# Kernel optimization log

Hardware: AMD Instinct MI355X
Metric: run time of the kernel (lower is better)

The kernel has to match this reference:

```python
import jax, jax.numpy as jnp
import numpy as np

DEGREE = 3
N_KNOTS = 5

def _bspline_basis(x, t_ext, degree):
    """Vectorized Cox-de Boor. x: (..., ), t_ext: (m,) extended knots.
    Returns (..., m-1-degree) degree-`degree` basis values."""
    xe = x[..., None]
    # order-0 indicator basis: (..., m-1)
    B = ((xe >= t_ext[:-1]) & (xe < t_ext[1:])).astype(x.dtype)
    for p in range(1, degree + 1):
        left_den = t_ext[p:-1] - t_ext[:-(p + 1)]
        right_den = t_ext[p + 1:] - t_ext[1:-p]
        left = jnp.where(left_den > 0,
                         (xe - t_ext[:-(p + 1)]) / jnp.where(left_den > 0, left_den, 1.0),
                         0.0) * B[..., :-1]
        right = jnp.where(right_den > 0,
                          (t_ext[p + 1:] - xe) / jnp.where(right_den > 0, right_den, 1.0),
                          0.0) * B[..., 1:]
        B = left + right
    return B

def setup_inputs() -> dict:
    key = jax.random.key(0)
    k1, k2, k3, k4 = jax.random.split(key, 4)
    batch, input_dim, out_dim = 16384, 4096, 64
    n_coeff = N_KNOTS - DEGREE  # 2
    return {
        "x": jax.random.normal(k1, (batch, input_dim), dtype=jnp.float32),
        "c": jax.random.normal(k2, (input_dim, out_dim, n_coeff), dtype=jnp.float32),
        "ws": jax.random.normal(k3, (input_dim, out_dim), dtype=jnp.float32),
        "wb": jax.random.normal(k4, (input_dim, out_dim), dtype=jnp.float32),
    }

def reference(x, c, ws, wb):
    t = jnp.linspace(-1.0, 1.0, N_KNOTS, dtype=x.dtype)
    t_ext = jnp.concatenate([t, t[-1:]])  # pad so basis count == n_knots - degree
    # B: (batch, input_dim, n_coeff); basis depends only on x, shared knots
    B = _bspline_basis(x, t_ext, DEGREE)
    spline = jnp.einsum('bik,ijk->bj', B, c * ws[:, :, None])
    silu_mix = jax.nn.silu(x) @ wb  # sum_i wb[i,j] * x_i*sigmoid(x_i)
    return spline + silu_mix
```

## Files before the change

kernel.cpp:

```cpp
#include <hip/hip_runtime.h>
#include <hip/hip_bf16.h>
#include <stdint.h>

#define BATCH   16384
#define IN_DIM  4096
#define OUT_DIM 64
#define KI      64
#define KCH     (3*KI)
#define NCHUNK  (IN_DIM/KI)
#define SPLITK  4
#define CPB     (NCHUNK/SPLITK)
#define MTILES  (BATCH/64)
#define CHW     (OUT_DIM*KCH)

typedef __attribute__((ext_vector_type(8))) short   short8;
typedef __attribute__((ext_vector_type(4))) float   floatx4;
typedef __attribute__((ext_vector_type(4))) uint32_t uintx4;

static __device__ __forceinline__ unsigned short f2bf(float f) {
    union { float f; uint32_t u; } v; v.f = f;
    uint32_t r = v.u + 0x7FFFu + ((v.u >> 16) & 1u);
    return (unsigned short)(r >> 16);
}

static __device__ __forceinline__ uint32_t pk2bf(float lo, float hi) {
    union { float f; uint32_t u; } a, b;
    a.f = lo; b.f = hi;
    uint32_t ra = a.u + 0x7FFFu + ((a.u >> 16) & 1u);
    uint32_t rb = b.u + 0x7FFFu + ((b.u >> 16) & 1u);
    return (ra >> 16) | (rb & 0xFFFF0000u);
}

static __device__ __forceinline__ void kan_features(float xv, float& b0, float& b1, float& sl) {
    float ax = fabsf(xv);
    float a2 = ax*ax;
    float om = 1.0f - ax;
    float inner = __builtin_fmaf(__builtin_fmaf(4.0f, ax, -4.0f), a2, (2.0f/3.0f));
    float outer = (om*om) * (om * (4.0f/3.0f));
    b0 = (ax < 0.5f) ? inner : outer;
    b0 = (ax < 1.0f) ? b0 : 0.0f;
    float c3  = (xv < 0.0f) ? (4.0f/3.0f) : (-14.0f/3.0f);
    float mid = __builtin_fmaf(__builtin_fmaf(__builtin_fmaf(c3, xv, 2.0f), xv, 1.0f), xv, (1.0f/6.0f));
    float hi  = __builtin_fmaf(__builtin_fmaf(__builtin_fmaf(22.0f, xv, -48.0f), xv, 30.0f), xv, -4.0f) * (1.0f/3.0f);
    b1 = (xv < 0.5f) ? mid : hi;
    b1 = (xv >= -0.5f && xv < 1.0f) ? b1 : 0.0f;
    float e = __expf(-xv);
    sl = xv * __builtin_amdgcn_rcpf(1.0f + e);
}

__global__ __launch_bounds__(256) void kan_prep(
        const float* __restrict__ c, const float* __restrict__ ws,
        const float* __restrict__ wb, unsigned short* __restrict__ Wt) {
    int idx = blockIdx.x * 256 + threadIdx.x;
    int row = idx >> 9;
    int i   = (idx & 511) << 3;
    int j   = row / 3;
    int t   = row - j*3;
    int ci  = i >> 6, il0 = i & 63;
    unsigned short pk[8];
    #pragma unroll
    for (int e = 0; e < 8; e++) {
        int ii = i + e;
        float v;
        if (t < 2) v = c[(size_t)ii*(OUT_DIM*2) + j*2 + t] * ws[(size_t)ii*OUT_DIM + j];
        else       v = wb[(size_t)ii*OUT_DIM + j];
        pk[e] = f2bf(v);
    }
    uintx4 d;
    d[0] = pk[0] | ((uint32_t)pk[1] << 16);
    d[1] = pk[2] | ((uint32_t)pk[3] << 16);
    d[2] = pk[4] | ((uint32_t)pk[5] << 16);
    d[3] = pk[6] | ((uint32_t)pk[7] << 16);
    int g = j*24 + (((t << 3) | (il0 >> 3)) ^ (j & 7));
    *(uintx4*)(Wt + (size_t)ci*CHW + g*8) = d;
}

__global__ __launch_bounds__(256, 4) void kan_main_pre(
    const float* __restrict__ x, const unsigned short* __restrict__ Wt,
    float* __restrict__ pbuf)
{
    __shared__ unsigned short Bs[CHW];

    const int tid  = threadIdx.x;
    const int wave = tid >> 6;
    const int lane = tid & 63;
    const int m    = lane & 15;
    const int q    = lane >> 4;
    const int mt   = blockIdx.x & (MTILES - 1);
    const int kh   = blockIdx.x >> 8;
    const int row0 = mt * 64;
    const int r    = row0 + wave*16 + m;
    const float* xrow = x + (size_t)r * IN_DIM;

    floatx4 acc[4] = {};

    const int i00 = kh * CPB * KI;
    floatx4 xv[4];
    xv[0] = *(const floatx4*)(xrow + i00 + q*8);
    xv[1] = *(const floatx4*)(xrow + i00 + q*8 + 4);
    xv[2] = *(const floatx4*)(xrow + i00 + 32 + q*8);
    xv[3] = *(const floatx4*)(xrow + i00 + 32 + q*8 + 4);

    for (int cc = 0; cc < CPB; cc++) {
        const int ci = kh * CPB + cc;
        const int i0 = ci * KI;

        const int inx = (cc + 1 < CPB) ? (i0 + KI) : i0;
        floatx4 xvn[4];
        xvn[0] = *(const floatx4*)(xrow + inx + q*8);
        xvn[1] = *(const floatx4*)(xrow + inx + q*8 + 4);
        xvn[2] = *(const floatx4*)(xrow + inx + 32 + q*8);
        xvn[3] = *(const floatx4*)(xrow + inx + 32 + q*8 + 4);

        uintx4 afu[6];
        #pragma unroll
        for (int g = 0; g < 2; g++) {
            #pragma unroll
            for (int w = 0; w < 4; w++) {
                float v0 = xv[g*2 + (w >> 1)][(w & 1)*2 + 0];
                float v1 = xv[g*2 + (w >> 1)][(w & 1)*2 + 1];
                float b00, b10, sl0, b01, b11, sl1;
                kan_features(v0, b00, b10, sl0);
                kan_features(v1, b01, b11, sl1);
                afu[0 + g][w] = pk2bf(b00, b01);
                afu[2 + g][w] = pk2bf(b10, b11);
                afu[4 + g][w] = pk2bf(sl0, sl1);
            }
        }

        __syncthreads();

        const unsigned short* gW = Wt + (size_t)ci * CHW;
        #pragma unroll
        for (int p = 0; p < 6; p++) {
            int g0 = p*256 + wave*64;
            __builtin_amdgcn_global_load_lds(
                (__attribute__((address_space(1))) void*)(gW + (size_t)(g0 + lane)*8),
                (__attribute__((address_space(3))) void*)(Bs + (size_t)g0*8),
                16, 0, 0);
        }

        __syncthreads();

        #pragma unroll
        for (int s = 0; s < 6; s++) {
            const int kb = (s >> 1)*8 + (s & 1)*4 + q;
            #pragma unroll
            for (int n = 0; n < 4; n++) {
                const int j = n*16 + m;
                short8 bf = *(const short8*)&Bs[j*KCH + ((kb ^ (j & 7)) << 3)];
                acc[n] = __builtin_amdgcn_mfma_f32_16x16x32_bf16(
                    __builtin_bit_cast(short8, afu[s]), bf, acc[n], 0, 0, 0);
            }
        }

        xv[0] = xvn[0]; xv[1] = xvn[1]; xv[2] = xvn[2]; xv[3] = xvn[3];
    }

    float* pb = pbuf + (((size_t)kh*MTILES + mt)*4)*256*4;
    #pragma unroll
    for (int n = 0; n < 4; n++)
        *(floatx4*)(pb + ((size_t)n*256 + tid)*4) = acc[n];
}

__global__ __launch_bounds__(256) void kan_reduce(
    const float* __restrict__ pbuf, float* __restrict__ out)
{
    const int mt   = blockIdx.x;
    const int tid  = threadIdx.x;
    const int wave = tid >> 6;
    const int lane = tid & 63;
    const int m    = lane & 15;
    const int q    = lane >> 4;
    #pragma unroll
    for (int n = 0; n < 4; n++) {
        floatx4 s = {};
        #pragma unroll
        for (int p = 0; p < SPLITK; p++) {
            floatx4 v = *(const floatx4*)(pbuf +
                ((((size_t)p*MTILES + mt)*4 + n)*256 + tid)*4);
            s += v;
        }
        #pragma unroll
        for (int reg = 0; reg < 4; reg++) {
            int orow = mt*64 + wave*16 + q*4 + reg;
            out[(size_t)orow*OUT_DIM + n*16 + m] = s[reg];
        }
    }
}

__global__ __launch_bounds__(256, 4) void kan_main_fb(
    const float* __restrict__ x, const float* __restrict__ c,
    const float* __restrict__ ws, const float* __restrict__ wb,
    float* __restrict__ out)
{
    __shared__ unsigned short Bs[CHW];
    const int tid  = threadIdx.x;
    const int wave = tid >> 6;
    const int lane = tid & 63;
    const int m    = lane & 15;
    const int q    = lane >> 4;
    const int mt   = blockIdx.x & (MTILES - 1);
    const int kh   = blockIdx.x >> 8;
    const int row0 = mt * 64;
    const int r    = row0 + wave*16 + m;
    const float* xrow = x + (size_t)r * IN_DIM;
    floatx4 acc[4] = {};
    for (int cc = 0; cc < CPB; cc++) {
        const int i0 = (kh * CPB + cc) * KI;
        floatx4 xv[4];
        xv[0] = *(const floatx4*)(xrow + i0 + q*8);
        xv[1] = *(const floatx4*)(xrow + i0 + q*8 + 4);
        xv[2] = *(const floatx4*)(xrow + i0 + 32 + q*8);
        xv[3] = *(const floatx4*)(xrow + i0 + 32 + q*8 + 4);
        uintx4 afu[6];
        #pragma unroll
        for (int g = 0; g < 2; g++) {
            #pragma unroll
            for (int w = 0; w < 4; w++) {
                float v0 = xv[g*2 + (w >> 1)][(w & 1)*2 + 0];
                float v1 = xv[g*2 + (w >> 1)][(w & 1)*2 + 1];
                float b00, b10, sl0, b01, b11, sl1;
                kan_features(v0, b00, b10, sl0);
                kan_features(v1, b01, b11, sl1);
                afu[0 + g][w] = pk2bf(b00, b01);
                afu[2 + g][w] = pk2bf(b10, b11);
                afu[4 + g][w] = pk2bf(sl0, sl1);
            }
        }
        __syncthreads();
        #pragma unroll
        for (int p = 0; p < 16; p++) {
            int idx = tid + p*256;
            int j = idx & 63, i = idx >> 6;
            int gi = i0 + i;
            const float* cp = c + ((size_t)gi*OUT_DIM + j)*2;
            float c0 = cp[0], c1 = cp[1];
            float sw = ws[(size_t)gi*OUT_DIM + j];
            float b  = wb[(size_t)gi*OUT_DIM + j];
            int jx = j & 7;
            Bs[j*KCH + ((0*8 + (i>>3)) ^ jx)*8 + (i&7)] = f2bf(c0*sw);
            Bs[j*KCH + ((1*8 + (i>>3)) ^ jx)*8 + (i&7)] = f2bf(c1*sw);
            Bs[j*KCH + ((2*8 + (i>>3)) ^ jx)*8 + (i&7)] = f2bf(b);
        }
        __syncthreads();
        #pragma unroll
        for (int s = 0; s < 6; s++) {
            const int kb = (s >> 1)*8 + (s & 1)*4 + q;
            #pragma unroll
            for (int n = 0; n < 4; n++) {
                const int j = n*16 + m;
                short8 bf = *(const short8*)&Bs[j*KCH + ((kb ^ (j & 7)) << 3)];
                acc[n] = __builtin_amdgcn_mfma_f32_16x16x32_bf16(
                    __builtin_bit_cast(short8, afu[s]), bf, acc[n], 0, 0, 0);
            }
        }
    }
    #pragma unroll
    for (int n = 0; n < 4; n++)
        #pragma unroll
        for (int reg = 0; reg < 4; reg++) {
            int orow = row0 + wave*16 + q*4 + reg;
            atomicAdd(&out[(size_t)orow*OUT_DIM + n*16 + m], acc[n][reg]);
        }
}

extern "C" void kernel_launch(void* const* d_in, const int* in_sizes, int n_in,
                              void* d_out, int out_size, void* d_ws, size_t ws_size,
                              hipStream_t stream) {
    const float* x  = (const float*)d_in[0];
    const float* c  = (const float*)d_in[1];
    const float* ws = (const float*)d_in[2];
    const float* wb = (const float*)d_in[3];
    float* out = (float*)d_out;

    const size_t part_bytes = (size_t)SPLITK * BATCH * OUT_DIM * sizeof(float);
    const size_t wt_bytes   = (size_t)NCHUNK * CHW * sizeof(unsigned short);
    if (ws_size >= part_bytes + wt_bytes) {
        float* pbuf = (float*)d_ws;
        unsigned short* Wt = (unsigned short*)((char*)d_ws + part_bytes);
        kan_prep<<<384, 256, 0, stream>>>(c, ws, wb, Wt);
        kan_main_pre<<<MTILES * SPLITK, 256, 0, stream>>>(x, Wt, pbuf);
        kan_reduce<<<MTILES, 256, 0, stream>>>(pbuf, out);
    } else {
        hipMemsetAsync(d_out, 0, (size_t)out_size * sizeof(float), stream);
        kan_main_fb<<<MTILES * SPLITK, 256, 0, stream>>>(x, c, ws, wb, out);
    }
}
```

Measured before the change: 411.3 us.

## Double-buffer weight chunks via async LDS loads with smaller K-chunks and split-K 8

The main kernel now processes 32-wide input chunks with split-K raised to 8, and double-buffers the pre-packed weight chunk in LDS. The next chunk's global_load_lds is issued before the MFMA work on the current one, leaving one barrier per iteration instead of two. The weight layout uses a padded stride of 13 granules per output column instead of the XOR swizzle, occupancy is raised to 6 blocks, and the basis math clamps inputs rather than adding range selects. The cost is a partial-sum buffer twice as large, a longer reduce, and more blocks.

```diff
diff --git a/kernel.cpp b/kernel.cpp
--- a/kernel.cpp
+++ b/kernel.cpp
@@ -5,12 +5,19 @@
 #define BATCH   16384
 #define IN_DIM  4096
 #define OUT_DIM 64
+#define MTILES  (BATCH/64)
+
+#define KI2     32
+#define NCH2    (IN_DIM/KI2)
+#define SPLITK  8
+#define CPB2    (NCH2/SPLITK)
+#define GRAN2   (OUT_DIM*13)
+#define CH2W    (GRAN2*8)
+
 #define KI      64
 #define KCH     (3*KI)
 #define NCHUNK  (IN_DIM/KI)
-#define SPLITK  4
-#define CPB     (NCHUNK/SPLITK)
-#define MTILES  (BATCH/64)
+#define FCPB    16
 #define CHW     (OUT_DIM*KCH)
 
 typedef __attribute__((ext_vector_type(8))) short   short8;
@@ -32,18 +39,18 @@
 }
 
 static __device__ __forceinline__ void kan_features(float xv, float& b0, float& b1, float& sl) {
-    float ax = fabsf(xv);
-    float a2 = ax*ax;
-    float om = 1.0f - ax;
-    float inner = __builtin_fmaf(__builtin_fmaf(4.0f, ax, -4.0f), a2, (2.0f/3.0f));
+    float ax  = fabsf(xv);
+    float axc = fminf(ax, 1.0f);
+    float a2  = axc*axc;
+    float om  = 1.0f - axc;
+    float inner = __builtin_fmaf(__builtin_fmaf(4.0f, axc, -4.0f), a2, (2.0f/3.0f));
     float outer = (om*om) * (om * (4.0f/3.0f));
-    b0 = (ax < 0.5f) ? inner : outer;
-    b0 = (ax < 1.0f) ? b0 : 0.0f;
-    float c3  = (xv < 0.0f) ? (4.0f/3.0f) : (-14.0f/3.0f);
-    float mid = __builtin_fmaf(__builtin_fmaf(__builtin_fmaf(c3, xv, 2.0f), xv, 1.0f), xv, (1.0f/6.0f));
-    float hi  = __builtin_fmaf(__builtin_fmaf(__builtin_fmaf(22.0f, xv, -48.0f), xv, 30.0f), xv, -4.0f) * (1.0f/3.0f);
-    b1 = (xv < 0.5f) ? mid : hi;
-    b1 = (xv >= -0.5f && xv < 1.0f) ? b1 : 0.0f;
+    b0 = (axc < 0.5f) ? inner : outer;
+    float xc  = fminf(fmaxf(xv, -0.5f), 1.0f);
+    float c3  = (xc < 0.0f) ? (4.0f/3.0f) : (-14.0f/3.0f);
+    float mid = __builtin_fmaf(__builtin_fmaf(__builtin_fmaf(c3, xc, 2.0f), xc, 1.0f), xc, (1.0f/6.0f));
+    float hi  = __builtin_fmaf(__builtin_fmaf(__builtin_fmaf(22.0f, xc, -48.0f), xc, 30.0f), xc, -4.0f) * (1.0f/3.0f);
+    b1 = (xc < 0.5f) ? mid : hi;
     float e = __expf(-xv);
     sl = xv * __builtin_amdgcn_rcpf(1.0f + e);
 }
@@ -56,7 +63,8 @@
     int i   = (idx & 511) << 3;
     int j   = row / 3;
     int t   = row - j*3;
-    int ci  = i >> 6, il0 = i & 63;
+    int ci  = i >> 5;
+    int ig  = (i & 31) >> 3;
     unsigned short pk[8];
     #pragma unroll
     for (int e = 0; e < 8; e++) {
@@ -71,15 +79,15 @@
     d[1] = pk[2] | ((uint32_t)pk[3] << 16);
     d[2] = pk[4] | ((uint32_t)pk[5] << 16);
     d[3] = pk[6] | ((uint32_t)pk[7] << 16);
-    int g = j*24 + (((t << 3) | (il0 >> 3)) ^ (j & 7));
-    *(uintx4*)(Wt + (size_t)ci*CHW + g*8) = d;
-}
-
-__global__ __launch_bounds__(256, 4) void kan_main_pre(
+    int g = j*13 + t*4 + ig;
+    *(uintx4*)(Wt + (size_t)ci*CH2W + (size_t)g*8) = d;
+}
+
+__global__ __launch_bounds__(256, 6) void kan_main_pre(
     const float* __restrict__ x, const unsigned short* __restrict__ Wt,
     float* __restrict__ pbuf)
 {
-    __shared__ unsigned short Bs[CHW];
+    __shared__ unsigned short Bs[2][CH2W];
 
     const int tid  = threadIdx.x;
     const int wave = tid >> 6;
@@ -91,27 +99,140 @@
     const int row0 = mt * 64;
     const int r    = row0 + wave*16 + m;
     const float* xrow = x + (size_t)r * IN_DIM;
+    const int ci0 = kh * CPB2;
 
     floatx4 acc[4] = {};
 
-    const int i00 = kh * CPB * KI;
-    floatx4 xv[4];
-    xv[0] = *(const floatx4*)(xrow + i00 + q*8);
-    xv[1] = *(const floatx4*)(xrow + i00 + q*8 + 4);
-    xv[2] = *(const floatx4*)(xrow + i00 + 32 + q*8);
-    xv[3] = *(const floatx4*)(xrow + i00 + 32 + q*8 + 4);
-
-    for (int cc = 0; cc < CPB; cc++) {
-        const int ci = kh * CPB + cc;
-        const int i0 = ci * KI;
-
-        const int inx = (cc + 1 < CPB) ? (i0 + KI) : i0;
-        floatx4 xvn[4];
-        xvn[0] = *(const floatx4*)(xrow + inx + q*8);
-        xvn[1] = *(const floatx4*)(xrow + inx + q*8 + 4);
-        xvn[2] = *(const floatx4*)(xrow + inx + 32 + q*8);
-        xvn[3] = *(const floatx4*)(xrow + inx + 32 + q*8 + 4);
-
+    floatx4 xv0 = *(const floatx4*)(xrow + ci0*KI2 + q*8);
+    floatx4 xv1 = *(const floatx4*)(xrow + ci0*KI2 + q*8 + 4);
+
+    {
+        const unsigned short* gW = Wt + (size_t)ci0 * CH2W;
+        #pragma unroll
+        for (int p = 0; p < 3; p++) {
+            int g0 = p*256 + wave*64;
+            __builtin_amdgcn_global_load_lds(
+                (__attribute__((address_space(1))) void*)(gW + (size_t)(g0 + lane)*8),
+                (__attribute__((address_space(3))) void*)(&Bs[0][0] + (size_t)g0*8),
+                16, 0, 0);
+        }
+        if (tid < 64)
+            __builtin_amdgcn_global_load_lds(
+                (__attribute__((address_space(1))) void*)(gW + (size_t)(768 + lane)*8),
+                (__attribute__((address_space(3))) void*)(&Bs[0][0] + (size_t)768*8),
+                16, 0, 0);
+    }
+    __syncthreads();
+
+    for (int cc = 0; cc < CPB2; cc++) {
+        const int buf = cc & 1;
+        const int ci  = ci0 + cc;
+
+        if (cc + 1 < CPB2) {
+            const unsigned short* gW = Wt + (size_t)(ci + 1) * CH2W;
+            #pragma unroll
+            for (int p = 0; p < 3; p++) {
+                int g0 = p*256 + wave*64;
+                __builtin_amdgcn_global_load_lds(
+                    (__attribute__((address_space(1))) void*)(gW + (size_t)(g0 + lane)*8),
+                    (__attribute__((address_space(3))) void*)(&Bs[buf^1][0] + (size_t)g0*8),
+                    16, 0, 0);
+            }
+            if (tid < 64)
+                __builtin_amdgcn_global_load_lds(
+                    (__attribute__((address_space(1))) void*)(gW + (size_t)(768 + lane)*8),
+                    (__attribute__((address_space(3))) void*)(&Bs[buf^1][0] + (size_t)768*8),
+                    16, 0, 0);
+        }
+
+        const int inx = (cc + 1 < CPB2) ? (ci + 1)*KI2 : ci*KI2;
+        floatx4 xn0 = *(const floatx4*)(xrow + inx + q*8);
+        floatx4 xn1 = *(const floatx4*)(xrow + inx + q*8 + 4);
+
+        uintx4 afu[3];
+        #pragma unroll
+        for (int w = 0; w < 4; w++) {
+            float v0 = (w < 2) ? xv0[w*2]     : xv1[(w-2)*2];
+            float v1 = (w < 2) ? xv0[w*2 + 1] : xv1[(w-2)*2 + 1];
+            float b00, b10, s0, b01, b11, s1;
+            kan_features(v0, b00, b10, s0);
+            kan_features(v1, b01, b11, s1);
+            afu[0][w] = pk2bf(b00, b01);
+            afu[1][w] = pk2bf(b10, b11);
+            afu[2][w] = pk2bf(s0, s1);
+        }
+
+        #pragma unroll
+        for (int t = 0; t < 3; t++) {
+            #pragma unroll
+            for (int n = 0; n < 4; n++) {
+                const int j = n*16 + m;
+                short8 bf = *(const short8*)&Bs[buf][(size_t)(j*13 + t*4 + q)*8];
+                acc[n] = __builtin_amdgcn_mfma_f32_16x16x32_bf16(
+                    __builtin_bit_cast(short8, afu[t]), bf, acc[n], 0, 0, 0);
+            }
+        }
+
+        xv0 = xn0; xv1 = xn1;
+        __syncthreads();
+    }
+
+    float* pb = pbuf + (((size_t)kh*MTILES + mt)*4)*1024;
+    #pragma unroll
+    for (int n = 0; n < 4; n++)
+        *(floatx4*)(pb + ((size_t)n*256 + tid)*4) = acc[n];
+}
+
+__global__ __launch_bounds__(256) void kan_reduce(
+    const float* __restrict__ pbuf, float* __restrict__ out)
+{
+    const int mt   = blockIdx.x;
+    const int tid  = threadIdx.x;
+    const int wave = tid >> 6;
+    const int lane = tid & 63;
+    const int m    = lane & 15;
+    const int q    = lane >> 4;
+    #pragma unroll
+    for (int n = 0; n < 4; n++) {
+        floatx4 s = {};
+        #pragma unroll
+        for (int p = 0; p < SPLITK; p++) {
+            floatx4 v = *(const floatx4*)(pbuf +
+                (((size_t)p*MTILES + mt)*4 + n)*1024 + (size_t)tid*4);
+            s += v;
+        }
+        #pragma unroll
+        for (int reg = 0; reg < 4; reg++) {
+            int orow = mt*64 + wave*16 + q*4 + reg;
+            out[(size_t)orow*OUT_DIM + n*16 + m] = s[reg];
+        }
+    }
+}
+
+__global__ __launch_bounds__(256, 4) void kan_main_fb(
+    const float* __restrict__ x, const float* __restrict__ c,
+    const float* __restrict__ ws, const float* __restrict__ wb,
+    float* __restrict__ out)
+{
+    __shared__ unsigned short Bsf[CHW];
+    const int tid  = threadIdx.x;
+    const int wave = tid >> 6;
+    const int lane = tid & 63;
+    const int m    = lane & 15;
+    const int q    = lane >> 4;
+    const int mt   = blockIdx.x & (MTILES - 1);
+    const int kh   = blockIdx.x >> 8;
+    const int row0 = mt * 64;
+    const int r    = row0 + wave*16 + m;
+    const float* xrow = x + (size_t)r * IN_DIM;
+    floatx4 acc[4] = {};
+    for (int cc = 0; cc < FCPB; cc++) {
+        const int i0 = (kh * FCPB + cc) * KI;
+        floatx4 xv[4];
+        xv[0] = *(const floatx4*)(xrow + i0 + q*8);
+        xv[1] = *(const floatx4*)(xrow + i0 + q*8 + 4);
+        xv[2] = *(const floatx4*)(xrow + i0 + 32 + q*8);
+        xv[3] = *(const floatx4*)(xrow + i0 + 32 + q*8 + 4);
         uintx4 afu[6];
         #pragma unroll
         for (int g = 0; g < 2; g++) {
@@ -127,107 +248,6 @@
                 afu[4 + g][w] = pk2bf(sl0, sl1);
             }
         }
-
-        __syncthreads();
-
-        const unsigned short* gW = Wt + (size_t)ci * CHW;
-        #pragma unroll
-        for (int p = 0; p < 6; p++) {
-            int g0 = p*256 + wave*64;
-            __builtin_amdgcn_global_load_lds(
-                (__attribute__((address_space(1))) void*)(gW + (size_t)(g0 + lane)*8),
-                (__attribute__((address_space(3))) void*)(Bs + (size_t)g0*8),
-                16, 0, 0);
-        }
-
-        __syncthreads();
-
-        #pragma unroll
-        for (int s = 0; s < 6; s++) {
-            const int kb = (s >> 1)*8 + (s & 1)*4 + q;
-            #pragma unroll
-            for (int n = 0; n < 4; n++) {
-                const int j = n*16 + m;
-                short8 bf = *(const short8*)&Bs[j*KCH + ((kb ^ (j & 7)) << 3)];
-                acc[n] = __builtin_amdgcn_mfma_f32_16x16x32_bf16(
-                    __builtin_bit_cast(short8, afu[s]), bf, acc[n], 0, 0, 0);
-            }
-        }
-
-        xv[0] = xvn[0]; xv[1] = xvn[1]; xv[2] = xvn[2]; xv[3] = xvn[3];
-    }
-
-    float* pb = pbuf + (((size_t)kh*MTILES + mt)*4)*256*4;
-    #pragma unroll
-    for (int n = 0; n < 4; n++)
-        *(floatx4*)(pb + ((size_t)n*256 + tid)*4) = acc[n];
-}
-
-__global__ __launch_bounds__(256) void kan_reduce(
-    const float* __restrict__ pbuf, float* __restrict__ out)
-{
-    const int mt   = blockIdx.x;
-    const int tid  = threadIdx.x;
-    const int wave = tid >> 6;
-    const int lane = tid & 63;
-    const int m    = lane & 15;
-    const int q    = lane >> 4;
-    #pragma unroll
-    for (int n = 0; n < 4; n++) {
-        floatx4 s = {};
-        #pragma unroll
-        for (int p = 0; p < SPLITK; p++) {
-            floatx4 v = *(const floatx4*)(pbuf +
-                ((((size_t)p*MTILES + mt)*4 + n)*256 + tid)*4);
-            s += v;
-        }
-        #pragma unroll
-        for (int reg = 0; reg < 4; reg++) {
-            int orow = mt*64 + wave*16 + q*4 + reg;
-            out[(size_t)orow*OUT_DIM + n*16 + m] = s[reg];
-        }
-    }
-}
-
-__global__ __launch_bounds__(256, 4) void kan_main_fb(
-    const float* __restrict__ x, const float* __restrict__ c,
-    const float* __restrict__ ws, const float* __restrict__ wb,
-    float* __restrict__ out)
-{
-    __shared__ unsigned short Bs[CHW];
-    const int tid  = threadIdx.x;
-    const int wave = tid >> 6;
-    const int lane = tid & 63;
-    const int m    = lane & 15;
-    const int q    = lane >> 4;
-    const int mt   = blockIdx.x & (MTILES - 1);
-    const int kh   = blockIdx.x >> 8;
-    const int row0 = mt * 64;
-    const int r    = row0 + wave*16 + m;
-    const float* xrow = x + (size_t)r * IN_DIM;
-    floatx4 acc[4] = {};
-    for (int cc = 0; cc < CPB; cc++) {
-        const int i0 = (kh * CPB + cc) * KI;
-        floatx4 xv[4];
-        xv[0] = *(const floatx4*)(xrow + i0 + q*8);
-        xv[1] = *(const floatx4*)(xrow + i0 + q*8 + 4);
-        xv[2] = *(const floatx4*)(xrow + i0 + 32 + q*8);
-        xv[3] = *(const floatx4*)(xrow + i0 + 32 + q*8 + 4);
-        uintx4 afu[6];
-        #pragma unroll
-        for (int g = 0; g < 2; g++) {
-            #pragma unroll
-            for (int w = 0; w < 4; w++) {
-                float v0 = xv[g*2 + (w >> 1)][(w & 1)*2 + 0];
-                float v1 = xv[g*2 + (w >> 1)][(w & 1)*2 + 1];
-                float b00, b10, sl0, b01, b11, sl1;
-                kan_features(v0, b00, b10, sl0);
-                kan_features(v1, b01, b11, sl1);
-                afu[0 + g][w] = pk2bf(b00, b01);
-                afu[2 + g][w] = pk2bf(b10, b11);
-                afu[4 + g][w] = pk2bf(sl0, sl1);
-            }
-        }
         __syncthreads();
         #pragma unroll
         for (int p = 0; p < 16; p++) {
@@ -239,9 +259,9 @@
             float sw = ws[(size_t)gi*OUT_DIM + j];
             float b  = wb[(size_t)gi*OUT_DIM + j];
             int jx = j & 7;
-            Bs[j*KCH + ((0*8 + (i>>3)) ^ jx)*8 + (i&7)] = f2bf(c0*sw);
-            Bs[j*KCH + ((1*8 + (i>>3)) ^ jx)*8 + (i&7)] = f2bf(c1*sw);
-            Bs[j*KCH + ((2*8 + (i>>3)) ^ jx)*8 + (i&7)] = f2bf(b);
+            Bsf[j*KCH + ((0*8 + (i>>3)) ^ jx)*8 + (i&7)] = f2bf(c0*sw);
+            Bsf[j*KCH + ((1*8 + (i>>3)) ^ jx)*8 + (i&7)] = f2bf(c1*sw);
+            Bsf[j*KCH + ((2*8 + (i>>3)) ^ jx)*8 + (i&7)] = f2bf(b);
         }
         __syncthreads();
         #pragma unroll
@@ -250,7 +270,7 @@
             #pragma unroll
             for (int n = 0; n < 4; n++) {
                 const int j = n*16 + m;
-                short8 bf = *(const short8*)&Bs[j*KCH + ((kb ^ (j & 7)) << 3)];
+                short8 bf = *(const short8*)&Bsf[j*KCH + ((kb ^ (j & 7)) << 3)];
                 acc[n] = __builtin_amdgcn_mfma_f32_16x16x32_bf16(
                     __builtin_bit_cast(short8, afu[s]), bf, acc[n], 0, 0, 0);
             }
@@ -275,7 +295,7 @@
     float* out = (float*)d_out;
 
     const size_t part_bytes = (size_t)SPLITK * BATCH * OUT_DIM * sizeof(float);
-    const size_t wt_bytes   = (size_t)NCHUNK * CHW * sizeof(unsigned short);
+    const size_t wt_bytes   = (size_t)NCH2 * CH2W * sizeof(unsigned short);
     if (ws_size >= part_bytes + wt_bytes) {
         float* pbuf = (float*)d_ws;
         unsigned short* Wt = (unsigned short*)((char*)d_ws + part_bytes);
@@ -284,6 +304,6 @@
         kan_reduce<<<MTILES, 256, 0, stream>>>(pbuf, out);
     } else {
         hipMemsetAsync(d_out, 0, (size_t)out_size * sizeof(float), stream);
-        kan_main_fb<<<MTILES * SPLITK, 256, 0, stream>>>(x, c, ws, wb, out);
-    }
-}
+        kan_main_fb<<<MTILES * 4, 256, 0, stream>>>(x, c, ws, wb, out);
+    }
+}
```

Result: faster. 402.0 us (-2.3%).
